# Optimization experiments

Hardware: AMD Instinct MI355X
Metric: run time of the kernel (lower is better)

The kernel has to match this reference:

```python
import jax, jax.numpy as jnp
import numpy as np

D, VH, DFF, NL, VOCAB, NH, NKV, HD, R, SCALE = 4096, 1024, 14336, 2, 32000, 32, 8, 128, 8, 4.0
B, NIMG, T = 2, 257, 511
S = NIMG + T

def _rmsnorm(x, w, eps=1e-5):
    v = jnp.mean(jnp.square(x), axis=-1, keepdims=True)
    return x * jax.lax.rsqrt(v + eps) * w

def _lora(x, W, A, Bm):
    # base (dequantized NF4 equivalent) matmul + low-rank LoRA path, scaling = alpha/r
    base = jnp.einsum('...d,od->...o', x, W)
    low = jnp.einsum('...r,or->...o', jnp.einsum('...d,rd->...r', x, A), Bm)
    return base + low * SCALE

def _rope_tables(s):
    inv = 1.0 / (10000.0 ** (jnp.arange(0, HD, 2, dtype=jnp.float32) / HD))
    ang = jnp.arange(s, dtype=jnp.float32)[:, None] * inv[None, :]
    c, sn = jnp.cos(ang), jnp.sin(ang)
    return jnp.concatenate([c, c], -1), jnp.concatenate([sn, sn], -1)

def _apply_rope(x, cos, sin):
    rot = jnp.concatenate([-x[..., HD // 2:], x[..., :HD // 2]], -1)
    return x * cos + rot * sin

def _forward(image_embeds, proj_W, proj_b, embed, ln1, ln2, ln_f, Wq, Aq, Bq, Wk, Ak, Bk, Wv, Av, Bv, Wo, Ao, Bo, Wg, Ag, Bg, Wu, Au, Bu, Wd, Ad, Bd, input_ids, attention_mask):
    b = image_embeds.shape[0]
    img = jnp.einsum('bsv,dv->bsd', image_embeds, proj_W) + proj_b  # projector
    txt = embed[input_ids]                                          # token embedding lookup
    h = jnp.concatenate([img, txt], axis=1)                         # (B, S, D)
    s = h.shape[1]
    cos, sin = _rope_tables(s)
    allow = jnp.tril(jnp.ones((s, s), bool))[None, None] & (attention_mask[:, None, None, :] > 0)
    for i in range(NL):
        x = _rmsnorm(h, ln1[i])
        q = _lora(x, Wq[i], Aq[i], Bq[i]).reshape(b, s, NH, HD).transpose(0, 2, 1, 3)
        k = _lora(x, Wk[i], Ak[i], Bk[i]).reshape(b, s, NKV, HD).transpose(0, 2, 1, 3)
        v = _lora(x, Wv[i], Av[i], Bv[i]).reshape(b, s, NKV, HD).transpose(0, 2, 1, 3)
        q = _apply_rope(q, cos, sin)
        k = _apply_rope(k, cos, sin)
        k = jnp.repeat(k, NH // NKV, axis=1)  # GQA: expand kv heads
        v = jnp.repeat(v, NH // NKV, axis=1)
        scores = jnp.einsum('bhsd,bhtd->bhst', q, k) / jnp.sqrt(jnp.float32(HD))
        scores = jnp.where(allow, scores, jnp.float32(-1e30))
        attn = jnp.einsum('bhst,bhtd->bhsd', jax.nn.softmax(scores, axis=-1), v)
        attn = attn.transpose(0, 2, 1, 3).reshape(b, s, D)
        h = h + _lora(attn, Wo[i], Ao[i], Bo[i])
        x = _rmsnorm(h, ln2[i])
        h = h + _lora(jax.nn.silu(_lora(x, Wg[i], Ag[i], Bg[i])) * _lora(x, Wu[i], Au[i], Bu[i]), Wd[i], Ad[i], Bd[i])
    return _rmsnorm(h, ln_f)  # HF hidden_states[-1] is post final norm

def setup_inputs():
    key = jax.random.key(0)
    ks = iter(jax.random.split(key, 40))
    n = lambda shape, sc=0.02: jax.random.normal(next(ks), shape, jnp.float32) * sc
    return dict(
        image_embeds=jax.random.normal(next(ks), (B, NIMG, VH), jnp.float32),
        input_ids=jax.random.randint(next(ks), (B, T), 0, VOCAB),
        attention_mask=jnp.ones((B, S), jnp.int32),
        proj_W=n((D, VH)), proj_b=jnp.zeros((D,), jnp.float32),
        embed=n((VOCAB, D)),
        ln1=jnp.ones((NL, D), jnp.float32), ln2=jnp.ones((NL, D), jnp.float32), ln_f=jnp.ones((D,), jnp.float32),
        Wq=n((NL, D, D)), Aq=n((NL, R, D)), Bq=n((NL, D, R)),
        Wk=n((NL, NKV * HD, D)), Ak=n((NL, R, D)), Bk=n((NL, NKV * HD, R)),
        Wv=n((NL, NKV * HD, D)), Av=n((NL, R, D)), Bv=n((NL, NKV * HD, R)),
        Wo=n((NL, D, D)), Ao=n((NL, R, D)), Bo=n((NL, D, R)),
        Wg=n((NL, DFF, D)), Ag=n((NL, R, D)), Bg=n((NL, DFF, R)),
        Wu=n((NL, DFF, D)), Au=n((NL, R, D)), Bu=n((NL, DFF, R)),
        Wd=n((NL, D, DFF)), Ad=n((NL, R, DFF)), Bd=n((NL, D, R)),
    )

def reference(image_embeds, input_ids, attention_mask, proj_W, proj_b, embed, ln1, ln2, ln_f, Wq, Aq, Bq, Wk, Ak, Bk, Wv, Av, Bv, Wo, Ao, Bo, Wg, Ag, Bg, Wu, Au, Bu, Wd, Ad, Bd):
    return _forward(image_embeds, proj_W, proj_b, embed, ln1, ln2, ln_f, Wq, Aq, Bq, Wk, Ak, Bk, Wv, Av, Bv, Wo, Ao, Bo, Wg, Ag, Bg, Wu, Au, Bu, Wd, Ad, Bd, input_ids, attention_mask)
```

## Files before the change

### kernel.cpp

```cpp
#include <hip/hip_runtime.h>
#include <hip/hip_bf16.h>
#include <cstdint>
#include <cstddef>

typedef unsigned short u16;
typedef unsigned int u32;
typedef __attribute__((ext_vector_type(8))) short short8;
typedef __attribute__((ext_vector_type(4))) short short4v;
typedef __attribute__((ext_vector_type(4))) float f32x4;

__device__ __forceinline__ u16 f2bf(float f) {
  u32 u = __float_as_uint(f);
  u32 r = (u + 0x7FFFu + ((u >> 16) & 1u)) >> 16;
  return (u16)r;
}
__device__ __forceinline__ float bf2f(u16 u) {
  return __uint_as_float(((u32)u) << 16);
}
__device__ __forceinline__ short f2bf_hw(float f) {
  union { __hip_bfloat16 h; u16 u; } c;
  c.h = __float2bfloat16(f);
  return (short)c.u;
}

__device__ __forceinline__ void gload_lds16(const void* g, void* l) {
  __builtin_amdgcn_global_load_lds((const __attribute__((address_space(1))) void*)g,
                                   (__attribute__((address_space(3))) void*)l, 16, 0, 0);
}

__global__ __launch_bounds__(256) void convert_w_kernel(const float* __restrict__ src,
    u16* __restrict__ dst, long n8) {
  long stride = (long)gridDim.x * 256;
  for (long i = (long)blockIdx.x * 256 + threadIdx.x; i < n8; i += stride) {
    const float* p = src + i * 8;
    float4 v0 = *(const float4*)p;
    float4 v1 = *(const float4*)(p + 4);
    uint4 w;
    w.x = (u32)(u16)f2bf_hw(v0.x) | ((u32)(u16)f2bf_hw(v0.y) << 16);
    w.y = (u32)(u16)f2bf_hw(v0.z) | ((u32)(u16)f2bf_hw(v0.w) << 16);
    w.z = (u32)(u16)f2bf_hw(v1.x) | ((u32)(u16)f2bf_hw(v1.y) << 16);
    w.w = (u32)(u16)f2bf_hw(v1.z) | ((u32)(u16)f2bf_hw(v1.w) << 16);
    *(uint4*)(dst + i * 8) = w;
  }
}

struct GemmArgs {
  const u16* A; int M; int K; int lda;
  const float* W0; const float* LB0; int toff0;
  const float* W1; const float* LB1; int toff1;
  const float* W2; const float* LB2; int toff2;
  const u16* Wb0; const u16* Wb1; const u16* Wb2;
  int ldw;
  int seg1; int seg2;
  const float* t;
  const float* bias;
  const float* resid;
  float* outf; int ostride;
  u16* outb0; u16* outb1;
  int rowremap;
  float* outp;
};

template<int WMODE>
__global__ __launch_bounds__(256) void gemm_kernel(GemmArgs a) {
  __shared__ u16 Asm[128 * 64];
  __shared__ u16 BsmW[WMODE ? 128 * 64 : 128 * 128];
  const int tid = threadIdx.x;

  const int nwg = gridDim.x * gridDim.y;
  const int bid0 = blockIdx.y * gridDim.x + blockIdx.x;
  const int q = nwg >> 3, r = nwg & 7;
  const int xcd = bid0 & 7, pos = bid0 >> 3;
  const int nb = (xcd < r ? xcd * (q + 1) : r * (q + 1) + (xcd - r) * q) + pos;
  const int m0 = (nb % gridDim.x) * 128;
  const int n0 = (nb / gridDim.x) * 128;

  const float* W = a.W0; const u16* Wb = a.Wb0;
  const float* LB = a.LB0; int toff = a.toff0; int nbase = 0;
  if (a.seg2 && n0 >= a.seg2)      { W = a.W2; Wb = a.Wb2; LB = a.LB2; toff = a.toff2; nbase = a.seg2; }
  else if (a.seg1 && n0 >= a.seg1) { W = a.W1; Wb = a.Wb1; LB = a.LB1; toff = a.toff1; nbase = a.seg1; }
  const int koff = blockIdx.z * a.K;
  const u16* Ab = a.A + koff;
  const float* Wt = W + (size_t)(n0 - nbase) * a.ldw + koff;
  const u16* Wbt = Wb + (size_t)(n0 - nbase) * a.ldw + koff;

  const int lane = tid & 63, wid = tid >> 6;
  const int wr = wid >> 1, wcn = wid & 1;
  const int lrow = lane & 15, g = lane >> 4;
  const int arow = lane >> 3;
  const int aslot = (lane & 7) ^ arow;
  const int brow4 = lane >> 4;

  f32x4 acc[4][4] = {};

  auto dma_A = [&](int k0) {
#pragma unroll
    for (int i = 0; i < 4; i++) {
      int c = wid * 4 + i;
      const u16* src = Ab + (size_t)(m0 + c * 8 + arow) * a.lda + k0 + (aslot << 3);
      gload_lds16(src, &Asm[c * 512]);
    }
  };
  auto dma_B = [&](int k0) {
    if (WMODE) {
#pragma unroll
      for (int i = 0; i < 4; i++) {
        int c = wid * 4 + i;
        const u16* src = Wbt + (size_t)(c * 8 + arow) * a.ldw + k0 + (aslot << 3);
        gload_lds16(src, &BsmW[c * 512]);
      }
    } else {
      float* Bf = (float*)BsmW;
#pragma unroll
      for (int j = 0; j < 8; j++) {
        int rrow = wid * 32 + j * 4 + brow4;
        int sslot = (lane & 15) ^ (rrow & 7);
        const float* src = Wt + (size_t)rrow * a.ldw + k0 + (sslot << 2);
        gload_lds16(src, &Bf[(wid * 32 + j * 4) * 64]);
      }
    }
  };

  dma_A(0);
  dma_B(0);
  const int nk = a.K >> 6;
  for (int kt = 0; kt < nk; kt++) {
    __syncthreads();

    short8 af[4][2], bq[4][2];
#pragma unroll
    for (int mi = 0; mi < 4; mi++) {
      int row = wr * 64 + mi * 16 + lrow;
#pragma unroll
      for (int x = 0; x < 2; x++) {
        int s = x * 4 + g;
        af[mi][x] = *(const short8*)&Asm[row * 64 + ((s ^ (lrow & 7)) << 3)];
      }
    }
#pragma unroll
    for (int ni = 0; ni < 4; ni++) {
      int row = wcn * 64 + ni * 16 + lrow;
      if (WMODE) {
#pragma unroll
        for (int x = 0; x < 2; x++) {
          int s = x * 4 + g;
          bq[ni][x] = *(const short8*)&BsmW[row * 64 + ((s ^ (lrow & 7)) << 3)];
        }
      } else {
        const float* bp = (const float*)BsmW + row * 64;
        int m = row & 7;
#pragma unroll
        for (int x = 0; x < 2; x++) {
          int sg0 = x * 8 + g * 2;
          f32x4 lo = *(const f32x4*)(bp + ((sg0 ^ m) << 2));
          f32x4 hi = *(const f32x4*)(bp + (((sg0 + 1) ^ m) << 2));
          short8 sv;
          sv[0] = f2bf_hw(lo[0]); sv[1] = f2bf_hw(lo[1]);
          sv[2] = f2bf_hw(lo[2]); sv[3] = f2bf_hw(lo[3]);
          sv[4] = f2bf_hw(hi[0]); sv[5] = f2bf_hw(hi[1]);
          sv[6] = f2bf_hw(hi[2]); sv[7] = f2bf_hw(hi[3]);
          bq[ni][x] = sv;
        }
      }
    }

    asm volatile("s_waitcnt lgkmcnt(0)" ::: "memory");
    __builtin_amdgcn_sched_barrier(0);
    __builtin_amdgcn_s_barrier();
    __builtin_amdgcn_sched_barrier(0);
    if (kt + 1 < nk) {
      dma_A((kt + 1) << 6);
      dma_B((kt + 1) << 6);
    }
#pragma unroll
    for (int x = 0; x < 2; x++)
#pragma unroll
      for (int mi = 0; mi < 4; mi++)
#pragma unroll
        for (int ni = 0; ni < 4; ni++)
          acc[mi][ni] = __builtin_amdgcn_mfma_f32_16x16x32_bf16(af[mi][x], bq[ni][x], acc[mi][ni], 0, 0, 0);
  }

  if (a.outp) {
    float* op = a.outp + (size_t)blockIdx.z * (1536 * 4096);
#pragma unroll
    for (int mi = 0; mi < 4; mi++)
#pragma unroll
      for (int rr = 0; rr < 4; rr++) {
        int row = m0 + wr * 64 + mi * 16 + (g << 2) + rr;
#pragma unroll
        for (int ni = 0; ni < 4; ni++) {
          int n = n0 + wcn * 64 + ni * 16 + lrow;
          op[(size_t)row * a.ostride + n] = acc[mi][ni][rr];
        }
      }
    return;
  }
  const bool dolora = (a.t != nullptr);
  float lbv[4][8];
#pragma unroll
  for (int ni = 0; ni < 4; ni++) {
    if (dolora) {
      int cl = wcn * 64 + ni * 16 + lrow;
      const float* bp = LB + (size_t)(n0 - nbase + cl) * 8;
#pragma unroll
      for (int r2 = 0; r2 < 8; r2++) lbv[ni][r2] = bp[r2];
    }
  }
#pragma unroll
  for (int mi = 0; mi < 4; mi++) {
#pragma unroll
    for (int rr = 0; rr < 4; rr++) {
      int row = m0 + wr * 64 + mi * 16 + (g << 2) + rr;
      if (row >= a.M) continue;
      float tv[8];
      if (dolora) {
        const float* tp = a.t + row * 32 + toff;
#pragma unroll
        for (int r2 = 0; r2 < 8; r2++) tv[r2] = tp[r2];
      }
#pragma unroll
      for (int ni = 0; ni < 4; ni++) {
        int n = n0 + wcn * 64 + ni * 16 + lrow;
        float val = acc[mi][ni][rr];
        if (dolora) {
          float ds = 0.f;
#pragma unroll
          for (int r2 = 0; r2 < 8; r2++) ds += tv[r2] * lbv[ni][r2];
          val += 4.0f * ds;
        }
        if (a.bias)  val += a.bias[n];
        if (a.resid) val += a.resid[(size_t)row * 4096 + n];
        if (a.outf) {
          int orow = a.rowremap ? (row < 257 ? row : row + 511) : row;
          a.outf[(size_t)orow * a.ostride + n] = val;
        } else if (a.seg1 && n >= a.seg1) {
          a.outb1[(size_t)row * a.ostride + (n - a.seg1)] = f2bf(val);
        } else {
          a.outb0[(size_t)row * a.ostride + n] = f2bf(val);
        }
      }
    }
  }
}

__global__ __launch_bounds__(256) void combine_kernel(float* __restrict__ h,
    const float* __restrict__ p, const float* __restrict__ t,
    const float* __restrict__ LB) {
  const int row = blockIdx.x;
  float tv[8];
  const float* tp = t + row * 32;
#pragma unroll
  for (int r = 0; r < 8; r++) tv[r] = tp[r];
  const float* p1 = p + (size_t)1536 * 4096;
#pragma unroll
  for (int i = 0; i < 4; i++) {
    int base = threadIdx.x * 4 + i * 1024;
    size_t off = (size_t)row * 4096 + base;
    float4 hv = *(const float4*)(h + off);
    float4 a0 = *(const float4*)(p + off);
    float4 a1 = *(const float4*)(p1 + off);
    float o[4] = {hv.x + a0.x + a1.x, hv.y + a0.y + a1.y,
                  hv.z + a0.z + a1.z, hv.w + a0.w + a1.w};
#pragma unroll
    for (int j = 0; j < 4; j++) {
      const float* lb = LB + (size_t)(base + j) * 8;
      float ds = 0.f;
#pragma unroll
      for (int r = 0; r < 8; r++) ds += tv[r] * lb[r];
      o[j] += 4.0f * ds;
    }
    float4 ov; ov.x = o[0]; ov.y = o[1]; ov.z = o[2]; ov.w = o[3];
    *(float4*)(h + off) = ov;
  }
}

template<int NA>
__global__ __launch_bounds__(256) void lora_xa_kernel(const u16* __restrict__ X, int K,
    const float* A0, const float* A1, const float* A2, float* __restrict__ t) {
  const int m = blockIdx.x;
  const u16* xr = X + (size_t)m * K;
  float acc[NA * 8];
#pragma unroll
  for (int i = 0; i < NA * 8; i++) acc[i] = 0.f;
  const float* Ap[3] = {A0, A1, A2};
  for (int k = threadIdx.x * 8; k < K; k += 2048) {
    uint4 xv = *(const uint4*)(xr + k);
    float xf[8];
    xf[0] = bf2f((u16)(xv.x & 0xffff)); xf[1] = bf2f((u16)(xv.x >> 16));
    xf[2] = bf2f((u16)(xv.y & 0xffff)); xf[3] = bf2f((u16)(xv.y >> 16));
    xf[4] = bf2f((u16)(xv.z & 0xffff)); xf[5] = bf2f((u16)(xv.z >> 16));
    xf[6] = bf2f((u16)(xv.w & 0xffff)); xf[7] = bf2f((u16)(xv.w >> 16));
#pragma unroll
    for (int aa = 0; aa < NA; aa++) {
#pragma unroll
      for (int r = 0; r < 8; r++) {
        const float* ar = Ap[aa] + (size_t)r * K + k;
        float4 a0 = *(const float4*)ar;
        float4 a1 = *(const float4*)(ar + 4);
        acc[aa * 8 + r] += xf[0] * a0.x + xf[1] * a0.y + xf[2] * a0.z + xf[3] * a0.w
                         + xf[4] * a1.x + xf[5] * a1.y + xf[6] * a1.z + xf[7] * a1.w;
      }
    }
  }
  __shared__ float red[4][NA * 8];
#pragma unroll
  for (int i = 0; i < NA * 8; i++) {
    float v = acc[i];
#pragma unroll
    for (int o = 1; o < 64; o <<= 1) v += __shfl_xor(v, o);
    if ((threadIdx.x & 63) == 0) red[threadIdx.x >> 6][i] = v;
  }
  __syncthreads();
  if (threadIdx.x < NA * 8)
    t[m * 32 + threadIdx.x] = red[0][threadIdx.x] + red[1][threadIdx.x]
                            + red[2][threadIdx.x] + red[3][threadIdx.x];
}

__global__ __launch_bounds__(256) void rmsnorm_kernel(const float* __restrict__ h,
    const float* __restrict__ w, u16* outb, float* outf) {
  const int m = blockIdx.x;
  const float* row = h + (size_t)m * 4096;
  float4 v[4];
  float ss = 0.f;
#pragma unroll
  for (int i = 0; i < 4; i++) {
    v[i] = *(const float4*)(row + threadIdx.x * 4 + i * 1024);
    ss += v[i].x * v[i].x + v[i].y * v[i].y + v[i].z * v[i].z + v[i].w * v[i].w;
  }
#pragma unroll
  for (int o = 1; o < 64; o <<= 1) ss += __shfl_xor(ss, o);
  __shared__ float red[4];
  if ((threadIdx.x & 63) == 0) red[threadIdx.x >> 6] = ss;
  __syncthreads();
  ss = red[0] + red[1] + red[2] + red[3];
  float rs = rsqrtf(ss * (1.f / 4096.f) + 1e-5f);
#pragma unroll
  for (int i = 0; i < 4; i++) {
    int base = threadIdx.x * 4 + i * 1024;
    float4 wv = *(const float4*)(w + base);
    float o0 = v[i].x * rs * wv.x, o1 = v[i].y * rs * wv.y;
    float o2 = v[i].z * rs * wv.z, o3 = v[i].w * rs * wv.w;
    if (outb) {
      short4v sv; sv.x = (short)f2bf(o0); sv.y = (short)f2bf(o1);
      sv.z = (short)f2bf(o2); sv.w = (short)f2bf(o3);
      *(short4v*)(outb + (size_t)m * 4096 + base) = sv;
    } else {
      float4 ov; ov.x = o0; ov.y = o1; ov.z = o2; ov.w = o3;
      *(float4*)(outf + (size_t)m * 4096 + base) = ov;
    }
  }
}

__global__ void rope_tab_kernel(float2* __restrict__ tab) {
  int idx = blockIdx.x * 256 + threadIdx.x;
  int s = idx >> 6, i = idx & 63;
  float inv = __expf(-(float)i * (9.210340371976184f / 64.f));
  float ang = (float)s * inv;
  float sn, cs;
  sincosf(ang, &sn, &cs);
  float2 r; r.x = cs; r.y = sn;
  tab[idx] = r;
}

__global__ __launch_bounds__(256) void rope_apply_kernel(float* __restrict__ qkv,
    const float2* __restrict__ tab) {
  int m = blockIdx.x;
  int s = m % 768;
  float* rowp = qkv + (size_t)m * 6144;
  for (int idx = threadIdx.x; idx < 2560; idx += 256) {
    int head = idx >> 6, i = idx & 63;
    int col = (head < 32) ? head * 128 : 4096 + (head - 32) * 128;
    float2 cs = tab[s * 64 + i];
    float x0 = rowp[col + i], x1 = rowp[col + i + 64];
    rowp[col + i]      = x0 * cs.x - x1 * cs.y;
    rowp[col + i + 64] = x1 * cs.x + x0 * cs.y;
  }
}

__global__ __launch_bounds__(256) void attn_mfma_kernel(const float* __restrict__ qkv,
    const int* __restrict__ amask, u16* __restrict__ attn_bf) {
  __shared__ u16 Ks[4][32][40];
  __shared__ u16 Vt[128][40];
  __shared__ u16 Ps[4][16][40];
  const int b = blockIdx.z, hh = blockIdx.y, q0 = blockIdx.x * 64;
  const int kvh = hh >> 2;
  const int tid = threadIdx.x, lane = tid & 63, w = tid >> 6;
  const int lrow = lane & 15, g = lane >> 4;
  const float sc = 0.08838834764831845f;

  short8 qf[4];
  {
    const float* qp = qkv + ((size_t)(b * 768 + q0 + w * 16 + lrow)) * 6144 + hh * 128;
#pragma unroll
    for (int ks = 0; ks < 4; ks++) {
      float4 lo = *(const float4*)(qp + ks * 32 + g * 8);
      float4 hi = *(const float4*)(qp + ks * 32 + g * 8 + 4);
      short8 sv;
      sv[0] = f2bf_hw(lo.x * sc); sv[1] = f2bf_hw(lo.y * sc);
      sv[2] = f2bf_hw(lo.z * sc); sv[3] = f2bf_hw(lo.w * sc);
      sv[4] = f2bf_hw(hi.x * sc); sv[5] = f2bf_hw(hi.y * sc);
      sv[6] = f2bf_hw(hi.z * sc); sv[7] = f2bf_hw(hi.w * sc);
      qf[ks] = sv;
    }
  }

  f32x4 acco[8] = {};
  float mrun[4] = {-1e30f, -1e30f, -1e30f, -1e30f};
  float lrun[4] = {0.f, 0.f, 0.f, 0.f};
  const int ntile = (q0 >> 5) + 2;

  for (int kt = 0; kt < ntile; kt++) {
    const int k0 = kt * 32;
    __syncthreads();
#pragma unroll
    for (int i = 0; i < 4; i++) {
      int idx = i * 256 + tid;
      int r2 = idx >> 5, c4 = (idx & 31) << 2;
      const float* kp = qkv + ((size_t)(b * 768 + k0 + r2)) * 6144 + 4096 + kvh * 128 + c4;
      float4 kv = *(const float4*)kp;
      short4v ksv;
      ksv.x = f2bf_hw(kv.x); ksv.y = f2bf_hw(kv.y);
      ksv.z = f2bf_hw(kv.z); ksv.w = f2bf_hw(kv.w);
      *(short4v*)&Ks[c4 >> 5][r2][c4 & 31] = ksv;
      float4 vv = *(const float4*)(kp + 1024);
      Vt[c4 + 0][r2] = (u16)f2bf_hw(vv.x);
      Vt[c4 + 1][r2] = (u16)f2bf_hw(vv.y);
      Vt[c4 + 2][r2] = (u16)f2bf_hw(vv.z);
      Vt[c4 + 3][r2] = (u16)f2bf_hw(vv.w);
    }
    __syncthreads();

    f32x4 s0 = {}, s1 = {};
#pragma unroll
    for (int ks = 0; ks < 4; ks++) {
      short8 kb0 = *(const short8*)&Ks[ks][lrow][g * 8];
      short8 kb1 = *(const short8*)&Ks[ks][16 + lrow][g * 8];
      s0 = __builtin_amdgcn_mfma_f32_16x16x32_bf16(qf[ks], kb0, s0, 0, 0, 0);
      s1 = __builtin_amdgcn_mfma_f32_16x16x32_bf16(qf[ks], kb1, s1, 0, 0, 0);
    }
    const int key0 = k0 + lrow, key1 = k0 + 16 + lrow;
    const bool am0 = amask[b * 768 + key0] != 0;
    const bool am1 = amask[b * 768 + key1] != 0;
    float scl4[4];
#pragma unroll
    for (int rr = 0; rr < 4; rr++) {
      int qrow = q0 + w * 16 + g * 4 + rr;
      float v0 = (key0 <= qrow && am0) ? s0[rr] : -1e30f;
      float v1 = (key1 <= qrow && am1) ? s1[rr] : -1e30f;
      float m = fmaxf(v0, v1);
      m = fmaxf(m, __shfl_xor(m, 1));
      m = fmaxf(m, __shfl_xor(m, 2));
      m = fmaxf(m, __shfl_xor(m, 4));
      m = fmaxf(m, __shfl_xor(m, 8));
      float mnew = fmaxf(mrun[rr], m);
      float scl = __expf(mrun[rr] - mnew);
      float p0 = __expf(v0 - mnew);
      float p1 = __expf(v1 - mnew);
      float ls = p0 + p1;
      ls += __shfl_xor(ls, 1);
      ls += __shfl_xor(ls, 2);
      ls += __shfl_xor(ls, 4);
      ls += __shfl_xor(ls, 8);
      lrun[rr] = lrun[rr] * scl + ls;
      mrun[rr] = mnew;
      scl4[rr] = scl;
      Ps[w][g * 4 + rr][lrow]      = (u16)f2bf_hw(p0);
      Ps[w][g * 4 + rr][16 + lrow] = (u16)f2bf_hw(p1);
    }
#pragma unroll
    for (int nf = 0; nf < 8; nf++)
#pragma unroll
      for (int rr = 0; rr < 4; rr++) acco[nf][rr] *= scl4[rr];

    asm volatile("s_waitcnt lgkmcnt(0)" ::: "memory");
    __builtin_amdgcn_sched_barrier(0);
    short8 pa = *(const short8*)&Ps[w][lrow][g * 8];
#pragma unroll
    for (int nf = 0; nf < 8; nf++) {
      short8 vb = *(const short8*)&Vt[nf * 16 + lrow][g * 8];
      acco[nf] = __builtin_amdgcn_mfma_f32_16x16x32_bf16(pa, vb, acco[nf], 0, 0, 0);
    }
  }

#pragma unroll
  for (int rr = 0; rr < 4; rr++) {
    float inv = 1.f / lrun[rr];
    size_t orow = (size_t)(b * 768 + q0 + w * 16 + g * 4 + rr);
#pragma unroll
    for (int nf = 0; nf < 8; nf++)
      attn_bf[orow * 4096 + hh * 128 + nf * 16 + lrow] = f2bf(acco[nf][rr] * inv);
  }
}

__global__ void convert_img_kernel(const float* __restrict__ in, u16* __restrict__ out) {
  int idx = blockIdx.x * 256 + threadIdx.x;
  if (idx >= 81920) return;
  uint4 w = {0u, 0u, 0u, 0u};
  if (idx < 65792) {
    const float* p = in + (size_t)idx * 8;
    float4 v0 = *(const float4*)p;
    float4 v1 = *(const float4*)(p + 4);
    w.x = (u32)f2bf(v0.x) | ((u32)f2bf(v0.y) << 16);
    w.y = (u32)f2bf(v0.z) | ((u32)f2bf(v0.w) << 16);
    w.z = (u32)f2bf(v1.x) | ((u32)f2bf(v1.y) << 16);
    w.w = (u32)f2bf(v1.z) | ((u32)f2bf(v1.w) << 16);
  }
  *(uint4*)(out + (size_t)idx * 8) = w;
}

__global__ void embed_gather_kernel(const float* __restrict__ embed,
    const int* __restrict__ ids, float* __restrict__ h) {
  int row = blockIdx.x;
  int b = row / 511, tt = row % 511;
  int id = ids[b * 511 + tt];
  const float* src = embed + (size_t)id * 4096;
  float* dst = h + ((size_t)(b * 768 + 257 + tt)) * 4096;
  for (int i = threadIdx.x * 4; i < 4096; i += 1024)
    *(float4*)(dst + i) = *(const float4*)(src + i);
}

__global__ __launch_bounds__(256) void gu_combine_kernel(const u16* __restrict__ g,
    const u16* __restrict__ u, u16* __restrict__ x2) {
  size_t idx = (size_t)blockIdx.x * 256 + threadIdx.x;
  uint4 gv = *(const uint4*)(g + idx * 8);
  uint4 uv = *(const uint4*)(u + idx * 8);
  u32 gi[4] = {gv.x, gv.y, gv.z, gv.w};
  u32 ui[4] = {uv.x, uv.y, uv.z, uv.w};
  u32 oi[4];
#pragma unroll
  for (int i = 0; i < 4; i++) {
    float g0 = bf2f((u16)(gi[i] & 0xffff)), g1 = bf2f((u16)(gi[i] >> 16));
    float u0 = bf2f((u16)(ui[i] & 0xffff)), u1 = bf2f((u16)(ui[i] >> 16));
    float s0 = g0 / (1.f + __expf(-g0)) * u0;
    float s1 = g1 / (1.f + __expf(-g1)) * u1;
    oi[i] = (u32)f2bf(s0) | ((u32)f2bf(s1) << 16);
  }
  uint4 ov; ov.x = oi[0]; ov.y = oi[1]; ov.z = oi[2]; ov.w = oi[3];
  *(uint4*)(x2 + idx * 8) = ov;
}

extern "C" void kernel_launch(void* const* d_in, const int* in_sizes, int n_in,
                              void* d_out, int out_size, void* d_ws, size_t ws_size,
                              hipStream_t stream) {
  const float* image_embeds = (const float*)d_in[0];
  const int*   input_ids    = (const int*)d_in[1];
  const int*   amask        = (const int*)d_in[2];
  const float* proj_W = (const float*)d_in[3];
  const float* proj_b = (const float*)d_in[4];
  const float* embed  = (const float*)d_in[5];
  const float* ln1 = (const float*)d_in[6];
  const float* ln2 = (const float*)d_in[7];
  const float* ln_f = (const float*)d_in[8];
  const float* Wq = (const float*)d_in[9];
  const float* Aq = (const float*)d_in[10];
  const float* Bq = (const float*)d_in[11];
  const float* Wk = (const float*)d_in[12];
  const float* Ak = (const float*)d_in[13];
  const float* Bk = (const float*)d_in[14];
  const float* Wv = (const float*)d_in[15];
  const float* Av = (const float*)d_in[16];
  const float* Bv = (const float*)d_in[17];
  const float* Wo = (const float*)d_in[18];
  const float* Ao = (const float*)d_in[19];
  const float* Bo = (const float*)d_in[20];
  const float* Wg = (const float*)d_in[21];
  const float* Ag = (const float*)d_in[22];
  const float* Bg = (const float*)d_in[23];
  const float* Wu = (const float*)d_in[24];
  const float* Au = (const float*)d_in[25];
  const float* Bu = (const float*)d_in[26];
  const float* Wd = (const float*)d_in[27];
  const float* Ad = (const float*)d_in[28];
  const float* Bd = (const float*)d_in[29];
  (void)in_sizes; (void)n_in; (void)out_size;

  char* ws = (char*)d_ws;
  size_t off = 0;
  auto alloc = [&](size_t bytes) -> void* {
    void* p = ws + off; off += (bytes + 255) & ~(size_t)255; return p;
  };
  float* h       = (float*) alloc((size_t)1536 * 4096 * 4);
  u16*   xn      = (u16*)   alloc((size_t)1536 * 4096 * 2);
  float* qkv     = (float*) alloc((size_t)1536 * 6144 * 4);
  u16*   attn_bf = (u16*)   alloc((size_t)1536 * 4096 * 2);
  u16*   g_bf    = (u16*)   alloc((size_t)1536 * 14336 * 2);
  u16*   u_bf    = (u16*)   alloc((size_t)1536 * 14336 * 2);
  u16*   x2_bf   = (u16*)   alloc((size_t)1536 * 14336 * 2);
  float* t       = (float*) alloc((size_t)1536 * 32 * 4);
  float2* tab    = (float2*)alloc((size_t)768 * 64 * 8);
  u16*   img_bf  = (u16*)   alloc((size_t)640 * 1024 * 2);
  float* pc      = (float*) alloc((size_t)2 * 1536 * 4096 * 4);
  const size_t nQ = (size_t)2 * 4096 * 4096;
  const size_t nK = (size_t)2 * 1024 * 4096;
  const size_t nG = (size_t)2 * 14336 * 4096;
  u16* wq_b = (u16*)alloc(nQ * 2);
  u16* wk_b = (u16*)alloc(nK * 2);
  u16* wv_b = (u16*)alloc(nK * 2);
  u16* wo_b = (u16*)alloc(nQ * 2);
  u16* wg_b = (u16*)alloc(nG * 2);
  u16* wu_b = (u16*)alloc(nG * 2);
  u16* wd_b = (u16*)alloc(nG * 2);
  const bool use_bf = (off <= ws_size);

  dim3 blk(256);
  if (use_bf) {
    convert_w_kernel<<<dim3(2048), blk, 0, stream>>>(Wq, wq_b, (long)(nQ / 8));
    convert_w_kernel<<<dim3(1024), blk, 0, stream>>>(Wk, wk_b, (long)(nK / 8));
    convert_w_kernel<<<dim3(1024), blk, 0, stream>>>(Wv, wv_b, (long)(nK / 8));
    convert_w_kernel<<<dim3(2048), blk, 0, stream>>>(Wo, wo_b, (long)(nQ / 8));
    convert_w_kernel<<<dim3(2048), blk, 0, stream>>>(Wg, wg_b, (long)(nG / 8));
    convert_w_kernel<<<dim3(2048), blk, 0, stream>>>(Wu, wu_b, (long)(nG / 8));
    convert_w_kernel<<<dim3(2048), blk, 0, stream>>>(Wd, wd_b, (long)(nG / 8));
  }
  auto launch_gemm = [&](const GemmArgs& a, dim3 grid) {
    if (a.Wb0) gemm_kernel<1><<<grid, blk, 0, stream>>>(a);
    else       gemm_kernel<0><<<grid, blk, 0, stream>>>(a);
  };

  convert_img_kernel<<<dim3(320), blk, 0, stream>>>(image_embeds, img_bf);
  rope_tab_kernel<<<dim3(192), blk, 0, stream>>>(tab);

  {
    GemmArgs a = {};
    a.A = img_bf; a.M = 514; a.K = 1024; a.lda = 1024; a.ldw = 1024;
    a.W0 = proj_W;
    a.bias = proj_b;
    a.outf = h; a.ostride = 4096; a.rowremap = 1;
    launch_gemm(a, dim3(5, 32));
  }
  embed_gather_kernel<<<dim3(1022), blk, 0, stream>>>(embed, input_ids, h);

  for (int l = 0; l < 2; l++) {
    const float* Wq_l = Wq + (size_t)l * 4096 * 4096;
    const float* Aq_l = Aq + (size_t)l * 8 * 4096;
    const float* Bq_l = Bq + (size_t)l * 4096 * 8;
    const float* Wk_l = Wk + (size_t)l * 1024 * 4096;
    const float* Ak_l = Ak + (size_t)l * 8 * 4096;
    const float* Bk_l = Bk + (size_t)l * 1024 * 8;
    const float* Wv_l = Wv + (size_t)l * 1024 * 4096;
    const float* Av_l = Av + (size_t)l * 8 * 4096;
    const float* Bv_l = Bv + (size_t)l * 1024 * 8;
    const float* Wo_l = Wo + (size_t)l * 4096 * 4096;
    const float* Ao_l = Ao + (size_t)l * 8 * 4096;
    const float* Bo_l = Bo + (size_t)l * 4096 * 8;
    const float* Wg_l = Wg + (size_t)l * 14336 * 4096;
    const float* Ag_l = Ag + (size_t)l * 8 * 4096;
    const float* Bg_l = Bg + (size_t)l * 14336 * 8;
    const float* Wu_l = Wu + (size_t)l * 14336 * 4096;
    const float* Au_l = Au + (size_t)l * 8 * 4096;
    const float* Bu_l = Bu + (size_t)l * 14336 * 8;
    const float* Wd_l = Wd + (size_t)l * 4096 * 14336;
    const float* Ad_l = Ad + (size_t)l * 8 * 14336;
    const float* Bd_l = Bd + (size_t)l * 4096 * 8;
    const u16* wq_bl = use_bf ? wq_b + (size_t)l * 4096 * 4096 : nullptr;
    const u16* wk_bl = use_bf ? wk_b + (size_t)l * 1024 * 4096 : nullptr;
    const u16* wv_bl = use_bf ? wv_b + (size_t)l * 1024 * 4096 : nullptr;
    const u16* wo_bl = use_bf ? wo_b + (size_t)l * 4096 * 4096 : nullptr;
    const u16* wg_bl = use_bf ? wg_b + (size_t)l * 14336 * 4096 : nullptr;
    const u16* wu_bl = use_bf ? wu_b + (size_t)l * 14336 * 4096 : nullptr;
    const u16* wd_bl = use_bf ? wd_b + (size_t)l * 14336 * 4096 : nullptr;

    rmsnorm_kernel<<<dim3(1536), blk, 0, stream>>>(h, ln1 + l * 4096, xn, (float*)nullptr);
    lora_xa_kernel<3><<<dim3(1536), blk, 0, stream>>>(xn, 4096, Aq_l, Ak_l, Av_l, t);
    {
      GemmArgs a = {};
      a.A = xn; a.M = 1536; a.K = 4096; a.lda = 4096; a.ldw = 4096;
      a.W0 = Wq_l; a.LB0 = Bq_l; a.toff0 = 0;
      a.W1 = Wk_l; a.LB1 = Bk_l; a.toff1 = 8;
      a.W2 = Wv_l; a.LB2 = Bv_l; a.toff2 = 16;
      a.Wb0 = wq_bl; a.Wb1 = wk_bl; a.Wb2 = wv_bl;
      a.seg1 = 4096; a.seg2 = 5120;
      a.t = t; a.outf = qkv; a.ostride = 6144;
      launch_gemm(a, dim3(12, 48));
    }
    rope_apply_kernel<<<dim3(1536), blk, 0, stream>>>(qkv, tab);
    attn_mfma_kernel<<<dim3(12, 32, 2), blk, 0, stream>>>(qkv, amask, attn_bf);
    lora_xa_kernel<1><<<dim3(1536), blk, 0, stream>>>(attn_bf, 4096, Ao_l,
        (const float*)nullptr, (const float*)nullptr, t);
    {
      GemmArgs a = {};
      a.A = attn_bf; a.M = 1536; a.K = 2048; a.lda = 4096; a.ldw = 4096;
      a.W0 = Wo_l; a.Wb0 = wo_bl;
      a.ostride = 4096; a.outp = pc;
      launch_gemm(a, dim3(12, 32, 2));
      combine_kernel<<<dim3(1536), blk, 0, stream>>>(h, pc, t, Bo_l);
    }
    rmsnorm_kernel<<<dim3(1536), blk, 0, stream>>>(h, ln2 + l * 4096, xn, (float*)nullptr);
    lora_xa_kernel<2><<<dim3(1536), blk, 0, stream>>>(xn, 4096, Ag_l, Au_l,
        (const float*)nullptr, t);
    {
      GemmArgs a = {};
      a.A = xn; a.M = 1536; a.K = 4096; a.lda = 4096; a.ldw = 4096;
      a.W0 = Wg_l; a.LB0 = Bg_l; a.toff0 = 0;
      a.W1 = Wu_l; a.LB1 = Bu_l; a.toff1 = 8;
      a.Wb0 = wg_bl; a.Wb1 = wu_bl;
      a.seg1 = 14336;
      a.t = t; a.outb0 = g_bf; a.outb1 = u_bf; a.ostride = 14336;
      launch_gemm(a, dim3(12, 224));
    }
    gu_combine_kernel<<<dim3(10752), blk, 0, stream>>>(g_bf, u_bf, x2_bf);
    lora_xa_kernel<1><<<dim3(1536), blk, 0, stream>>>(x2_bf, 14336, Ad_l,
        (const float*)nullptr, (const float*)nullptr, t);
    {
      GemmArgs a = {};
      a.A = x2_bf; a.M = 1536; a.K = 7168; a.lda = 14336; a.ldw = 14336;
      a.W0 = Wd_l; a.Wb0 = wd_bl;
      a.ostride = 4096; a.outp = pc;
      launch_gemm(a, dim3(12, 32, 2));
      combine_kernel<<<dim3(1536), blk, 0, stream>>>(h, pc, t, Bd_l);
    }
  }
  rmsnorm_kernel<<<dim3(1536), blk, 0, stream>>>(h, ln_f, (u16*)nullptr, (float*)d_out);
}
```

Measured before the change: 3.185 ms.

## Overlap weight bf16 conversion with preceding GEMMs via extra conversion blocks

Up front, only layer-0 Q/K/V weights are converted. Each later weight's fp32-to-bf16 conversion now runs in extra grid rows (16 y-blocks) appended to the GEMM launched just before that weight is needed. The goal is to hide the conversion memory traffic behind compute-bound GEMM work and drop the separate up-front conversion launches. The risk is that conversion blocks compete with GEMM tiles for bandwidth and CUs. Ordering relies on stream serialization, so each conversion must finish before the consuming GEMM starts.

```diff
diff --git a/kernel.cpp b/kernel.cpp
--- a/kernel.cpp
+++ b/kernel.cpp
@@ -44,6 +44,7 @@
   }
 }
 
+struct ConvJob { const float* src; u16* dst; long n8; };
 struct GemmArgs {
   const u16* A; int M; int K; int lda;
   const float* W0; const float* LB0; int toff0;
@@ -59,6 +60,8 @@
   u16* outb0; u16* outb1;
   int rowremap;
   float* outp;
+  int ny_main;
+  ConvJob cj[3];
 };
 
 template<int WMODE>
@@ -67,7 +70,33 @@
   __shared__ u16 BsmW[WMODE ? 128 * 64 : 128 * 128];
   const int tid = threadIdx.x;
 
-  const int nwg = gridDim.x * gridDim.y;
+  const int nym = a.ny_main;
+  if ((int)blockIdx.y >= nym) {
+    if (blockIdx.z != 0) return;
+    const long cb = (long)((int)blockIdx.y - nym) * gridDim.x + blockIdx.x;
+    const long cstr = (long)((int)gridDim.y - nym) * gridDim.x * 256;
+#pragma unroll
+    for (int j = 0; j < 3; j++) {
+      const float* src = a.cj[j].src;
+      if (!src) break;
+      u16* dst = a.cj[j].dst;
+      const long n8 = a.cj[j].n8;
+      for (long i = cb * 256 + tid; i < n8; i += cstr) {
+        const float* p = src + i * 8;
+        float4 v0 = *(const float4*)p;
+        float4 v1 = *(const float4*)(p + 4);
+        uint4 w;
+        w.x = (u32)(u16)f2bf_hw(v0.x) | ((u32)(u16)f2bf_hw(v0.y) << 16);
+        w.y = (u32)(u16)f2bf_hw(v0.z) | ((u32)(u16)f2bf_hw(v0.w) << 16);
+        w.z = (u32)(u16)f2bf_hw(v1.x) | ((u32)(u16)f2bf_hw(v1.y) << 16);
+        w.w = (u32)(u16)f2bf_hw(v1.z) | ((u32)(u16)f2bf_hw(v1.w) << 16);
+        *(uint4*)(dst + i * 8) = w;
+      }
+    }
+    return;
+  }
+
+  const int nwg = gridDim.x * nym;
   const int bid0 = blockIdx.y * gridDim.x + blockIdx.x;
   const int q = nwg >> 3, r = nwg & 7;
   const int xcd = bid0 & 7, pos = bid0 >> 3;
@@ -594,6 +623,7 @@
   const size_t nQ = (size_t)2 * 4096 * 4096;
   const size_t nK = (size_t)2 * 1024 * 4096;
   const size_t nG = (size_t)2 * 14336 * 4096;
+  const long nQl8 = 4096L * 4096 / 8, nKl8 = 1024L * 4096 / 8, nGl8 = 14336L * 4096 / 8;
   u16* wq_b = (u16*)alloc(nQ * 2);
   u16* wk_b = (u16*)alloc(nK * 2);
   u16* wv_b = (u16*)alloc(nK * 2);
@@ -602,16 +632,13 @@
   u16* wu_b = (u16*)alloc(nG * 2);
   u16* wd_b = (u16*)alloc(nG * 2);
   const bool use_bf = (off <= ws_size);
+  const int CONVY = 16;
 
   dim3 blk(256);
   if (use_bf) {
-    convert_w_kernel<<<dim3(2048), blk, 0, stream>>>(Wq, wq_b, (long)(nQ / 8));
-    convert_w_kernel<<<dim3(1024), blk, 0, stream>>>(Wk, wk_b, (long)(nK / 8));
-    convert_w_kernel<<<dim3(1024), blk, 0, stream>>>(Wv, wv_b, (long)(nK / 8));
-    convert_w_kernel<<<dim3(2048), blk, 0, stream>>>(Wo, wo_b, (long)(nQ / 8));
-    convert_w_kernel<<<dim3(2048), blk, 0, stream>>>(Wg, wg_b, (long)(nG / 8));
-    convert_w_kernel<<<dim3(2048), blk, 0, stream>>>(Wu, wu_b, (long)(nG / 8));
-    convert_w_kernel<<<dim3(2048), blk, 0, stream>>>(Wd, wd_b, (long)(nG / 8));
+    convert_w_kernel<<<dim3(512), blk, 0, stream>>>(Wq, wq_b, nQl8);
+    convert_w_kernel<<<dim3(256), blk, 0, stream>>>(Wk, wk_b, nKl8);
+    convert_w_kernel<<<dim3(256), blk, 0, stream>>>(Wv, wv_b, nKl8);
   }
   auto launch_gemm = [&](const GemmArgs& a, dim3 grid) {
     if (a.Wb0) gemm_kernel<1><<<grid, blk, 0, stream>>>(a);
@@ -627,6 +654,7 @@
     a.W0 = proj_W;
     a.bias = proj_b;
     a.outf = h; a.ostride = 4096; a.rowremap = 1;
+    a.ny_main = 32;
     launch_gemm(a, dim3(5, 32));
   }
   embed_gather_kernel<<<dim3(1022), blk, 0, stream>>>(embed, input_ids, h);
@@ -653,13 +681,13 @@
     const float* Wd_l = Wd + (size_t)l * 4096 * 14336;
     const float* Ad_l = Ad + (size_t)l * 8 * 14336;
     const float* Bd_l = Bd + (size_t)l * 4096 * 8;
-    const u16* wq_bl = use_bf ? wq_b + (size_t)l * 4096 * 4096 : nullptr;
-    const u16* wk_bl = use_bf ? wk_b + (size_t)l * 1024 * 4096 : nullptr;
-    const u16* wv_bl = use_bf ? wv_b + (size_t)l * 1024 * 4096 : nullptr;
-    const u16* wo_bl = use_bf ? wo_b + (size_t)l * 4096 * 4096 : nullptr;
-    const u16* wg_bl = use_bf ? wg_b + (size_t)l * 14336 * 4096 : nullptr;
-    const u16* wu_bl = use_bf ? wu_b + (size_t)l * 14336 * 4096 : nullptr;
-    const u16* wd_bl = use_bf ? wd_b + (size_t)l * 14336 * 4096 : nullptr;
+    u16* wq_bl = wq_b + (size_t)l * 4096 * 4096;
+    u16* wk_bl = wk_b + (size_t)l * 1024 * 4096;
+    u16* wv_bl = wv_b + (size_t)l * 1024 * 4096;
+    u16* wo_bl = wo_b + (size_t)l * 4096 * 4096;
+    u16* wg_bl = wg_b + (size_t)l * 14336 * 4096;
+    u16* wu_bl = wu_b + (size_t)l * 14336 * 4096;
+    u16* wd_bl = wd_b + (size_t)l * 14336 * 4096;
 
     rmsnorm_kernel<<<dim3(1536), blk, 0, stream>>>(h, ln1 + l * 4096, xn, (float*)nullptr);
     lora_xa_kernel<3><<<dim3(1536), blk, 0, stream>>>(xn, 4096, Aq_l, Ak_l, Av_l, t);
@@ -669,10 +697,17 @@
       a.W0 = Wq_l; a.LB0 = Bq_l; a.toff0 = 0;
       a.W1 = Wk_l; a.LB1 = Bk_l; a.toff1 = 8;
       a.W2 = Wv_l; a.LB2 = Bv_l; a.toff2 = 16;
-      a.Wb0 = wq_bl; a.Wb1 = wk_bl; a.Wb2 = wv_bl;
       a.seg1 = 4096; a.seg2 = 5120;
       a.t = t; a.outf = qkv; a.ostride = 6144;
-      launch_gemm(a, dim3(12, 48));
+      a.ny_main = 48;
+      dim3 grid(12, 48);
+      if (use_bf) {
+        a.Wb0 = wq_bl; a.Wb1 = wk_bl; a.Wb2 = wv_bl;
+        a.cj[0] = {Wo_l, wo_bl, nQl8};
+        a.cj[1] = {Wg_l, wg_bl, nGl8};
+        grid = dim3(12, 48 + CONVY);
+      }
+      launch_gemm(a, grid);
     }
     rope_apply_kernel<<<dim3(1536), blk, 0, stream>>>(qkv, tab);
     attn_mfma_kernel<<<dim3(12, 32, 2), blk, 0, stream>>>(qkv, amask, attn_bf);
@@ -681,9 +716,16 @@
     {
       GemmArgs a = {};
       a.A = attn_bf; a.M = 1536; a.K = 2048; a.lda = 4096; a.ldw = 4096;
-      a.W0 = Wo_l; a.Wb0 = wo_bl;
+      a.W0 = Wo_l;
       a.ostride = 4096; a.outp = pc;
-      launch_gemm(a, dim3(12, 32, 2));
+      a.ny_main = 32;
+      dim3 grid(12, 32, 2);
+      if (use_bf) {
+        a.Wb0 = wo_bl;
+        a.cj[0] = {Wu_l, wu_bl, nGl8};
+        grid = dim3(12, 32 + CONVY, 2);
+      }
+      launch_gemm(a, grid);
       combine_kernel<<<dim3(1536), blk, 0, stream>>>(h, pc, t, Bo_l);
     }
     rmsnorm_kernel<<<dim3(1536), blk, 0, stream>>>(h, ln2 + l * 4096, xn, (float*)nullptr);
@@ -694,10 +736,16 @@
       a.A = xn; a.M = 1536; a.K = 4096; a.lda = 4096; a.ldw = 4096;
       a.W0 = Wg_l; a.LB0 = Bg_l; a.toff0 = 0;
       a.W1 = Wu_l; a.LB1 = Bu_l; a.toff1 = 8;
-      a.Wb0 = wg_bl; a.Wb1 = wu_bl;
       a.seg1 = 14336;
       a.t = t; a.outb0 = g_bf; a.outb1 = u_bf; a.ostride = 14336;
-      launch_gemm(a, dim3(12, 224));
+      a.ny_main = 224;
+      dim3 grid(12, 224);
+      if (use_bf) {
+        a.Wb0 = wg_bl; a.Wb1 = wu_bl;
+        a.cj[0] = {Wd_l, wd_bl, nGl8};
+        grid = dim3(12, 224 + CONVY);
+      }
+      launch_gemm(a, grid);
     }
     gu_combine_kernel<<<dim3(10752), blk, 0, stream>>>(g_bf, u_bf, x2_bf);
     lora_xa_kernel<1><<<dim3(1536), blk, 0, stream>>>(x2_bf, 14336, Ad_l,
@@ -705,9 +753,20 @@
     {
       GemmArgs a = {};
       a.A = x2_bf; a.M = 1536; a.K = 7168; a.lda = 14336; a.ldw = 14336;
-      a.W0 = Wd_l; a.Wb0 = wd_bl;
+      a.W0 = Wd_l;
       a.ostride = 4096; a.outp = pc;
-      launch_gemm(a, dim3(12, 32, 2));
+      a.ny_main = 32;
+      dim3 grid(12, 32, 2);
+      if (use_bf) {
+        a.Wb0 = wd_bl;
+        if (l == 0) {
+          a.cj[0] = {Wq + (size_t)4096 * 4096, wq_b + (size_t)4096 * 4096, nQl8};
+          a.cj[1] = {Wk + (size_t)1024 * 4096, wk_b + (size_t)1024 * 4096, nKl8};
+          a.cj[2] = {Wv + (size_t)1024 * 4096, wv_b + (size_t)1024 * 4096, nKl8};
+          grid = dim3(12, 32 + CONVY, 2);
+        }
+      }
+      launch_gemm(a, grid);
       combine_kernel<<<dim3(1536), blk, 0, stream>>>(h, pc, t, Bd_l);
     }
   }
```

New measurement: 3.126 ms. About the same (-1.9%).
